# Optimization experiments

Measured on AMD Instinct MI355X. Metric: run time of the kernel, lower is better.

The kernel has to match this reference:

```python
import jax, jax.numpy as jnp
import numpy as np

# Model dims (match init_kwargs / input_specs)
T, N, E, F_IN, F_OUT, BW = 16, 50000, 131072, 64, 64, 3


def setup_inputs() -> dict:
    key = jax.random.key(0)
    ks = jax.random.split(key, 6)
    x = jax.random.normal(ks[0], (T, N, F_IN), dtype=jnp.float32)
    M = jax.random.normal(ks[1], (T, T), dtype=jnp.float32)
    adj_rows = jax.random.randint(ks[2], (T, E), 0, N, dtype=jnp.int32)
    adj_cols = jax.random.randint(ks[3], (T, E), 0, N, dtype=jnp.int32)
    adj_vals = jax.random.uniform(ks[4], (T, E), dtype=jnp.float32)
    lim = float(np.sqrt(6.0 / (F_IN + F_OUT)))  # xavier_uniform
    weight = jax.random.uniform(ks[5], (F_IN, F_OUT), minval=-lim, maxval=lim, dtype=jnp.float32)
    return {"x": x, "M": M, "adj_vals": adj_vals, "weight": weight,
            "adj_rows": adj_rows, "adj_cols": adj_cols}


def _spmm(vals, rows, cols, x):
    # COO sparse [N,N] @ dense [N,F]: gather source rows, scatter-add to dest rows.
    return jax.ops.segment_sum(vals[:, None] * x[cols], rows, num_segments=x.shape[0])


def reference(x, M, adj_vals, weight, adj_rows, adj_cols):
    Tn, Nn, F = x.shape
    # Xt = M @ X (full M, as in compute_AtXt)
    Xt = (M @ x.reshape(Tn, -1)).reshape(Tn, Nn, F)
    k_idx = jnp.arange(Tn)
    AtXt = jnp.zeros((Tn, Nn, F), dtype=x.dtype)
    # Banded combination: At[k] = sum_{d=0}^{BW-1, k-d>=0} M[k, k-d] * A[k-d]
    # so At[k] @ Xt[k] = sum_d M[k,k-d] * (A[k-d] @ Xt[k])  -- avoids materializing At.
    for d in range(BW):
        j = k_idx - d
        valid = j >= 0
        jc = jnp.maximum(j, 0)
        w = jnp.where(valid, M[k_idx, jc], 0.0)  # [T] banded weights
        contrib = jax.vmap(_spmm)(adj_vals[jc], adj_rows[jc], adj_cols[jc], Xt)  # [T,N,F]
        AtXt = AtXt + w[:, None, None] * contrib
    # dropout is identity in eval mode; final dense projection
    return AtXt @ weight  # [T, N, F_OUT]
```

## Files before the change

kernel.cpp:

```cpp
#include <hip/hip_runtime.h>

#define TT 16
#define NN 50000
#define FF 64
#define EE 131072
#define NEDGE (TT*EE)
#define RPB 32
#define NRANGE ((NN + RPB - 1) / RPB)
#define NSUB 8
#define BCAP 256
#define NBUCK (NRANGE*NSUB)
#define SLOTS (NSUB*BCAP)
#define EMAX 1791
#define TAILI (EMAX*2)
#define NTILES 6250
#define K1BLKS 1563
#define APPBLKS (NEDGE/256)

typedef __attribute__((ext_vector_type(8))) short bf16x8;
typedef __attribute__((ext_vector_type(4))) short bf16x4;
typedef __attribute__((ext_vector_type(4))) float f32x4;
typedef __attribute__((ext_vector_type(2))) int   i32x2;
typedef __attribute__((ext_vector_type(2))) unsigned u32x2;

__device__ __forceinline__ unsigned pack2bf(float a, float b) {
    unsigned ua = __float_as_uint(a) + 0x8000u;
    unsigned ub = __float_as_uint(b) + 0x8000u;
    return __builtin_amdgcn_perm(ub, ua, 0x07060302u);
}
__device__ __forceinline__ float lo16f(unsigned u) { return __uint_as_float(u << 16); }
__device__ __forceinline__ float hi16f(unsigned u) { return __uint_as_float(u & 0xFFFF0000u); }

union U8 { unsigned u[4]; bf16x8 v; };
union U4 { unsigned u[2]; bf16x4 v; };

__device__ __forceinline__ f32x4 mfma16x16x16bf16(bf16x4 a, bf16x4 b, f32x4 c) {
#if __has_builtin(__builtin_amdgcn_mfma_f32_16x16x16bf16_1k)
    return __builtin_amdgcn_mfma_f32_16x16x16bf16_1k(a, b, c, 0, 0, 0);
#elif __has_builtin(__builtin_amdgcn_mfma_f32_16x16x16_bf16)
    return __builtin_amdgcn_mfma_f32_16x16x16_bf16(a, b, c, 0, 0, 0);
#else
    f32x4 d;
    asm volatile("v_mfma_f32_16x16x16_bf16 %0, %1, %2, %3\n\ts_nop 7\n\ts_nop 7"
                 : "=&v"(d) : "v"(a), "v"(b), "v"(c));
    return d;
#endif
}

__global__ void k1_append(
    const float* __restrict__ x, const float* __restrict__ M,
    const float* __restrict__ W, unsigned short* __restrict__ Yt,
    const int* __restrict__ rows, const int* __restrict__ cols,
    const float* __restrict__ vals, int* __restrict__ bcnt,
    i32x2* __restrict__ btmp)
{
    __shared__ __align__(16) char lds[2][16384];

    if (blockIdx.x < K1BLKS) {
        const int tid  = threadIdx.x;
        const int wid  = tid >> 6;
        const int lane = tid & 63;
        const int col  = lane & 15;
        const int grp  = lane >> 4;

        bf16x8 bw[2][4];
#pragma unroll
        for (int q = 0; q < 2; ++q)
#pragma unroll
            for (int t = 0; t < 4; ++t) {
                U8 w8;
#pragma unroll
                for (int p = 0; p < 4; ++p)
                    w8.u[p] = pack2bf(W[(q*32 + grp*8 + 2*p)*FF + t*16 + col],
                                      W[(q*32 + grp*8 + 2*p + 1)*FF + t*16 + col]);
                bw[q][t] = w8.v;
            }

        U4 m4;
        m4.u[0] = pack2bf(M[col*16 + grp*4 + 0], M[col*16 + grp*4 + 1]);
        m4.u[1] = pack2bf(M[col*16 + grp*4 + 2], M[col*16 + grp*4 + 3]);
        const bf16x4 mf = m4.v;
        const f32x4 zero = {0.f, 0.f, 0.f, 0.f};

#define STAGE(tt, buf)                                                        \
        {                                                                     \
            const int nb_ = (tt)*8;                                           \
            char* L_ = lds[buf];                                              \
            _Pragma("unroll")                                                 \
            for (int q = 0; q < 4; ++q) {                                     \
                const int s_ = wid*4 + q;                                     \
                const float* src_ = x + (size_t)s_*NN*FF + (size_t)nb_*FF + lane*8; \
                float4 lo_ = *reinterpret_cast<const float4*>(src_);          \
                float4 hi_ = *reinterpret_cast<const float4*>(src_ + 4);      \
                U8 pk_;                                                       \
                pk_.u[0] = pack2bf(lo_.x, lo_.y); pk_.u[1] = pack2bf(lo_.z, lo_.w); \
                pk_.u[2] = pack2bf(hi_.x, hi_.y); pk_.u[3] = pack2bf(hi_.z, hi_.w); \
                const int byte_ = (s_*1024 + lane*16) ^ ((s_ & 7) << 4);      \
                *reinterpret_cast<bf16x8*>(L_ + byte_) = pk_.v;               \
            }                                                                 \
        }

        const int t0 = blockIdx.x*4;
        if (t0 < NTILES) STAGE(t0, 0)

#pragma unroll
        for (int i = 0; i < 4; ++i) {
            const int t = t0 + i;
            if (t >= NTILES) break;
            __syncthreads();
            if (i + 1 < 4 && t + 1 < NTILES) STAGE(t + 1, (i + 1) & 1)

            const char* L = lds[i & 1];
#pragma unroll
            for (int h = 0; h < 2; ++h) {
                const int nloc = wid*2 + h;
                const int node = t*8 + nloc;
                const int base = (col*1024 + nloc*128) ;
                const int sw = (col & 7) << 4;
                bf16x8 a0 = *reinterpret_cast<const bf16x8*>(L + ((base + grp*16) ^ sw));
                bf16x8 a1 = *reinterpret_cast<const bf16x8*>(L + ((base + 64 + grp*16) ^ sw));

                f32x4 acc[4];
#pragma unroll
                for (int t2 = 0; t2 < 4; ++t2) acc[t2] = zero;
#pragma unroll
                for (int t2 = 0; t2 < 4; ++t2)
                    acc[t2] = __builtin_amdgcn_mfma_f32_16x16x32_bf16(a0, bw[0][t2], acc[t2], 0, 0, 0);
#pragma unroll
                for (int t2 = 0; t2 < 4; ++t2)
                    acc[t2] = __builtin_amdgcn_mfma_f32_16x16x32_bf16(a1, bw[1][t2], acc[t2], 0, 0, 0);

#pragma unroll
                for (int t2 = 0; t2 < 4; ++t2) {
                    U4 pb;
                    pb.u[0] = pack2bf(acc[t2][0], acc[t2][1]);
                    pb.u[1] = pack2bf(acc[t2][2], acc[t2][3]);
                    f32x4 y = mfma16x16x16bf16(pb.v, mf, zero);
                    u32x2 st;
                    st[0] = pack2bf(y[0], y[1]);
                    st[1] = pack2bf(y[2], y[3]);
                    *reinterpret_cast<u32x2*>(Yt + (size_t)node*1024 + col*64 + t2*16 + grp*4) = st;
                }
            }
        }
#undef STAGE
    } else {
        const int i = (blockIdx.x - K1BLKS)*256 + threadIdx.x;
        const int r = rows[i];
        const int j = i >> 17;
        const int b = (r >> 5)*NSUB + (blockIdx.x & 7);
        const int pos = atomicAdd(&bcnt[b], 1);
        if (pos < BCAP) {
            i32x2 e;
            e[0] = cols[i] | (((r & 31)*16 + j) << 16);
            e[1] = __float_as_int(vals[i]);
            btmp[(size_t)b*BCAP + pos] = e;
        }
    }
}

__global__ __launch_bounds__(256) void sort_kernel(
    const int* __restrict__ bcnt, i32x2* __restrict__ btmp)
{
    __shared__ i32x2 sbuf[SLOTS];
    __shared__ int scnt[512], soff[512], scur[512], pscan[256];

    const int tid = threadIdx.x;
    const int blk = blockIdx.x;
    i32x2* region = btmp + (size_t)blk*SLOTS;

    scnt[tid] = 0; scnt[tid + 256] = 0;
    __syncthreads();

    int bc[NSUB]; i32x2 ent[NSUB];
#pragma unroll
    for (int s = 0; s < NSUB; ++s) {
        int c = bcnt[blk*NSUB + s];
        bc[s] = c < BCAP ? c : BCAP;
    }
#pragma unroll
    for (int s = 0; s < NSUB; ++s)
        if (tid < bc[s]) {
            ent[s] = region[s*BCAP + tid];
            atomicAdd(&scnt[((unsigned)ent[s][0]) >> 16], 1);
        }
    __syncthreads();

    const int a0 = scnt[2*tid], a1 = scnt[2*tid + 1];
    const int ps = a0 + a1;
    pscan[tid] = ps;
    __syncthreads();
    for (int o = 1; o < 256; o <<= 1) {
        int v = (tid >= o) ? pscan[tid - o] : 0;
        __syncthreads();
        pscan[tid] += v;
        __syncthreads();
    }
    const int excl = pscan[tid] - ps;
    soff[2*tid] = excl;      soff[2*tid + 1] = excl + a0;
    scur[2*tid] = excl;      scur[2*tid + 1] = excl + a0;
    __syncthreads();

#pragma unroll
    for (int s = 0; s < NSUB; ++s)
        if (tid < bc[s]) {
            const int key = ((unsigned)ent[s][0]) >> 16;
            const int pos = atomicAdd(&scur[key], 1);
            i32x2 se; se[0] = ent[s][0] & 0xFFFF; se[1] = ent[s][1];
            sbuf[pos] = se;
        }
    __syncthreads();

    const int total = soff[511] + scnt[511];
    const int lim = total < EMAX ? total : EMAX;
    for (int i = tid; i < lim; i += 256) region[i] = sbuf[i];
    int* tail = (int*)region + TAILI;
    tail[tid] = soff[tid];
    tail[tid + 256] = soff[tid + 256];
    if (tid == 0) tail[512] = lim;
}

template<int J>
__device__ __forceinline__ void k2_batch(int p0, int nj, int sbase, int esub, int fq,
    const i32x2* eb, const unsigned short* __restrict__ Yt,
    const float* __restrict__ M, f32x4* acc)
{
    const int p = p0 + esub;
    const bool act = p < nj;
    const int li = act ? (sbase + p) : 0;
    const i32x2 ent = eb[li];
    const float v = act ? __int_as_float(ent[1]) : 0.f;
    const int node = act ? ent[0] : 0;
    const unsigned short* yb = Yt + (size_t)node*1024 + J*64 + fq*4;
    {
        const u32x2 uv = *reinterpret_cast<const u32x2*>(yb);
        const float wv = M[J*17] * v;
        acc[J][0] = fmaf(wv, lo16f(uv[0]), acc[J][0]);
        acc[J][1] = fmaf(wv, hi16f(uv[0]), acc[J][1]);
        acc[J][2] = fmaf(wv, lo16f(uv[1]), acc[J][2]);
        acc[J][3] = fmaf(wv, hi16f(uv[1]), acc[J][3]);
    }
    if constexpr (J < 15) {
        const u32x2 uv = *reinterpret_cast<const u32x2*>(yb + 64);
        const float wv = M[J*17 + 16] * v;
        acc[J+1][0] = fmaf(wv, lo16f(uv[0]), acc[J+1][0]);
        acc[J+1][1] = fmaf(wv, hi16f(uv[0]), acc[J+1][1]);
        acc[J+1][2] = fmaf(wv, lo16f(uv[1]), acc[J+1][2]);
        acc[J+1][3] = fmaf(wv, hi16f(uv[1]), acc[J+1][3]);
    }
    if constexpr (J < 14) {
        const u32x2 uv = *reinterpret_cast<const u32x2*>(yb + 128);
        const float wv = M[J*17 + 32] * v;
        acc[J+2][0] = fmaf(wv, lo16f(uv[0]), acc[J+2][0]);
        acc[J+2][1] = fmaf(wv, hi16f(uv[0]), acc[J+2][1]);
        acc[J+2][2] = fmaf(wv, lo16f(uv[1]), acc[J+2][2]);
        acc[J+2][3] = fmaf(wv, hi16f(uv[1]), acc[J+2][3]);
    }
}

__global__ __launch_bounds__(256) void k2_gather(
    const unsigned short* __restrict__ Yt, const float* __restrict__ M,
    const i32x2* __restrict__ btmp, float* __restrict__ out)
{
    __shared__ i32x2 ebuf[4][128];
    const int tid  = threadIdx.x;
    const int wid  = tid >> 6;
    const int lane = tid & 63;
    const int esub = lane >> 4;
    const int fq   = lane & 15;
    const int r   = blockIdx.x*4 + wid;
    const int blk = r >> 5;
    const int rl  = r & 31;

    const i32x2* region = btmp + (size_t)blk*SLOTS;
    const int* tail = (const int*)region + TAILI;
    int o_l = 0;
    if (lane < 17) o_l = tail[rl*16 + lane];
    int off[17];
#pragma unroll
    for (int j = 0; j < 17; ++j) off[j] = __builtin_amdgcn_readlane(o_l, j);
    int ntot = off[16] - off[0];
    ntot = ntot < 128 ? ntot : 128;
    const i32x2* rowsrc = region + off[0];

    i32x2* eb = ebuf[wid];
    if (lane < ntot)      eb[lane]      = rowsrc[lane];
    if (lane + 64 < ntot) eb[lane + 64] = rowsrc[lane + 64];

    int c[16], sb[16];
#pragma unroll
    for (int j = 0; j < 16; ++j) {
        c[j]  = off[j+1] - off[j];
        sb[j] = off[j] - off[0];
    }

    f32x4 acc[16];
#pragma unroll
    for (int k = 0; k < 16; ++k) acc[k] = (f32x4){0.f, 0.f, 0.f, 0.f};

#define P1(J) k2_batch<J>(0, c[J], sb[J], esub, fq, eb, Yt, M, acc);
    P1(0)  P1(1)  P1(2)  P1(3)  P1(4)  P1(5)  P1(6)  P1(7)
    P1(8)  P1(9)  P1(10) P1(11) P1(12) P1(13) P1(14) P1(15)
#undef P1
#define P2(J) for (int p0 = 4; p0 < c[J]; p0 += 4) \
        k2_batch<J>(p0, c[J], sb[J], esub, fq, eb, Yt, M, acc);
    P2(0)  P2(1)  P2(2)  P2(3)  P2(4)  P2(5)  P2(6)  P2(7)
    P2(8)  P2(9)  P2(10) P2(11) P2(12) P2(13) P2(14) P2(15)
#undef P2

#pragma unroll
    for (int k = 0; k < 16; ++k) {
#pragma unroll
        for (int u = 0; u < 4; ++u) {
            acc[k][u] += __shfl_xor(acc[k][u], 16);
            acc[k][u] += __shfl_xor(acc[k][u], 32);
        }
    }
    if (esub == 0) {
#pragma unroll
        for (int k = 0; k < 16; ++k) {
            *reinterpret_cast<f32x4*>(out + ((size_t)k*NN + r)*FF + fq*4) = acc[k];
        }
    }
}

extern "C" void kernel_launch(void* const* d_in, const int* in_sizes, int n_in,
                              void* d_out, int out_size, void* d_ws, size_t ws_size,
                              hipStream_t stream) {
    (void)in_sizes; (void)n_in; (void)out_size; (void)ws_size;
    const float* x     = (const float*)d_in[0];
    const float* M     = (const float*)d_in[1];
    const float* avals = (const float*)d_in[2];
    const float* W     = (const float*)d_in[3];
    const int*   arows = (const int*)d_in[4];
    const int*   acols = (const int*)d_in[5];
    float* out = (float*)d_out;

    char* ws = (char*)d_ws;
    size_t o = 0;
    unsigned short* Yt = (unsigned short*)(ws + o); o += (size_t)TT*NN*FF*2;
    o = (o + 255) & ~(size_t)255;
    int* bcnt = (int*)(ws + o); o += (size_t)NBUCK*4;  o = (o + 255) & ~(size_t)255;
    i32x2* btmp = (i32x2*)(ws + o);

    (void)hipMemsetAsync(bcnt, 0, (size_t)NBUCK*4, stream);
    hipLaunchKernelGGL(k1_append, dim3(K1BLKS + APPBLKS), dim3(256), 0, stream,
                       x, M, W, Yt, arows, acols, avals, bcnt, btmp);
    hipLaunchKernelGGL(sort_kernel, dim3(NRANGE), dim3(256), 0, stream, bcnt, btmp);
    hipLaunchKernelGGL(k2_gather, dim3(12500), dim3(256), 0, stream, Yt, M, btmp, out);
}
```

Measured before the change: 329.4 us.

## Vectorize edge append to four edges per thread and schedule it first

The edge bucketing branch now handles four edges per thread with 128-bit loads of rows, cols and vals, cutting its block count from 8192 to 2048, and these blocks are placed ahead of the dense transform blocks in the grid. The dense branch drops LDS double buffering in favour of a single buffer with stage, sync, compute, sync, which halves shared memory per block and may raise occupancy but gives up overlap of global loads with MFMA work. The sub-bucket choice still depends on blockIdx.x & 7, so contention on the atomics changes with the new block grouping.

New measurement: 347.7 us. 1.06x slower.

```diff
diff --git a/kernel.cpp b/kernel.cpp
--- a/kernel.cpp
+++ b/kernel.cpp
@@ -14,8 +14,8 @@
 #define EMAX 1791
 #define TAILI (EMAX*2)
 #define NTILES 6250
+#define APP4BLKS 2048
 #define K1BLKS 1563
-#define APPBLKS (NEDGE/256)
 
 typedef __attribute__((ext_vector_type(8))) short bf16x8;
 typedef __attribute__((ext_vector_type(4))) short bf16x4;
@@ -54,9 +54,34 @@
     const float* __restrict__ vals, int* __restrict__ bcnt,
     i32x2* __restrict__ btmp)
 {
-    __shared__ __align__(16) char lds[2][16384];
-
-    if (blockIdx.x < K1BLKS) {
+    __shared__ __align__(16) char lds[16384];
+
+    if (blockIdx.x < APP4BLKS) {
+        const int i0 = blockIdx.x*1024 + threadIdx.x*4;
+        const int4 r4 = *reinterpret_cast<const int4*>(rows + i0);
+        const int4 c4 = *reinterpret_cast<const int4*>(cols + i0);
+        const float4 v4 = *reinterpret_cast<const float4*>(vals + i0);
+        int rr[4] = {r4.x, r4.y, r4.z, r4.w};
+        int cc[4] = {c4.x, c4.y, c4.z, c4.w};
+        float vv[4] = {v4.x, v4.y, v4.z, v4.w};
+        int pos[4], bb[4];
+#pragma unroll
+        for (int e = 0; e < 4; ++e) {
+            bb[e] = (rr[e] >> 5)*NSUB + (blockIdx.x & 7);
+            pos[e] = atomicAdd(&bcnt[bb[e]], 1);
+        }
+#pragma unroll
+        for (int e = 0; e < 4; ++e) {
+            if (pos[e] < BCAP) {
+                const int j = (i0 + e) >> 17;
+                i32x2 ent;
+                ent[0] = cc[e] | (((rr[e] & 31)*16 + j) << 16);
+                ent[1] = __float_as_int(vv[e]);
+                btmp[(size_t)bb[e]*BCAP + pos[e]] = ent;
+            }
+        }
+    } else {
+        const int blk  = blockIdx.x - APP4BLKS;
         const int tid  = threadIdx.x;
         const int wid  = tid >> 6;
         const int lane = tid & 63;
@@ -82,10 +107,9 @@
         const bf16x4 mf = m4.v;
         const f32x4 zero = {0.f, 0.f, 0.f, 0.f};
 
-#define STAGE(tt, buf)                                                        \
+#define STAGE(tt)                                                             \
         {                                                                     \
             const int nb_ = (tt)*8;                                           \
-            char* L_ = lds[buf];                                              \
             _Pragma("unroll")                                                 \
             for (int q = 0; q < 4; ++q) {                                     \
                 const int s_ = wid*4 + q;                                     \
@@ -96,29 +120,26 @@
                 pk_.u[0] = pack2bf(lo_.x, lo_.y); pk_.u[1] = pack2bf(lo_.z, lo_.w); \
                 pk_.u[2] = pack2bf(hi_.x, hi_.y); pk_.u[3] = pack2bf(hi_.z, hi_.w); \
                 const int byte_ = (s_*1024 + lane*16) ^ ((s_ & 7) << 4);      \
-                *reinterpret_cast<bf16x8*>(L_ + byte_) = pk_.v;               \
+                *reinterpret_cast<bf16x8*>(lds + byte_) = pk_.v;              \
             }                                                                 \
         }
 
-        const int t0 = blockIdx.x*4;
-        if (t0 < NTILES) STAGE(t0, 0)
-
+        const int t0 = blk*4;
 #pragma unroll
         for (int i = 0; i < 4; ++i) {
             const int t = t0 + i;
             if (t >= NTILES) break;
+            STAGE(t)
             __syncthreads();
-            if (i + 1 < 4 && t + 1 < NTILES) STAGE(t + 1, (i + 1) & 1)
-
-            const char* L = lds[i & 1];
+
 #pragma unroll
             for (int h = 0; h < 2; ++h) {
                 const int nloc = wid*2 + h;
                 const int node = t*8 + nloc;
-                const int base = (col*1024 + nloc*128) ;
+                const int base = col*1024 + nloc*128;
                 const int sw = (col & 7) << 4;
-                bf16x8 a0 = *reinterpret_cast<const bf16x8*>(L + ((base + grp*16) ^ sw));
-                bf16x8 a1 = *reinterpret_cast<const bf16x8*>(L + ((base + 64 + grp*16) ^ sw));
+                bf16x8 a0 = *reinterpret_cast<const bf16x8*>(lds + ((base + grp*16) ^ sw));
+                bf16x8 a1 = *reinterpret_cast<const bf16x8*>(lds + ((base + 64 + grp*16) ^ sw));
 
                 f32x4 acc[4];
 #pragma unroll
@@ -142,20 +163,9 @@
                     *reinterpret_cast<u32x2*>(Yt + (size_t)node*1024 + col*64 + t2*16 + grp*4) = st;
                 }
             }
+            __syncthreads();
         }
 #undef STAGE
-    } else {
-        const int i = (blockIdx.x - K1BLKS)*256 + threadIdx.x;
-        const int r = rows[i];
-        const int j = i >> 17;
-        const int b = (r >> 5)*NSUB + (blockIdx.x & 7);
-        const int pos = atomicAdd(&bcnt[b], 1);
-        if (pos < BCAP) {
-            i32x2 e;
-            e[0] = cols[i] | (((r & 31)*16 + j) << 16);
-            e[1] = __float_as_int(vals[i]);
-            btmp[(size_t)b*BCAP + pos] = e;
-        }
     }
 }
 
@@ -344,7 +354,7 @@
     i32x2* btmp = (i32x2*)(ws + o);
 
     (void)hipMemsetAsync(bcnt, 0, (size_t)NBUCK*4, stream);
-    hipLaunchKernelGGL(k1_append, dim3(K1BLKS + APPBLKS), dim3(256), 0, stream,
+    hipLaunchKernelGGL(k1_append, dim3(APP4BLKS + K1BLKS), dim3(256), 0, stream,
                        x, M, W, Yt, arows, acols, avals, bcnt, btmp);
     hipLaunchKernelGGL(sort_kernel, dim3(NRANGE), dim3(256), 0, stream, bcnt, btmp);
     hipLaunchKernelGGL(k2_gather, dim3(12500), dim3(256), 0, stream, Yt, M, btmp, out);
```

## Split gather kernel into two launches over output time halves

Applied to the files above, without the earlier changes.

The gather kernel, which kept 16 output-time accumulators per lane, is split into two templated launches that each produce 8 output time steps. Each launch processes only the source time steps that feed its half, with time steps 6 and 7 read by both. The aim is to lower register pressure and raise occupancy. In exchange, edge lists and offsets are read twice, overlapping source rows are gathered twice, and there is an extra launch.

Measured after the change: 421.0 us. +27.8%, slower.

```diff
diff --git a/kernel.cpp b/kernel.cpp
--- a/kernel.cpp
+++ b/kernel.cpp
@@ -115,7 +115,7 @@
             for (int h = 0; h < 2; ++h) {
                 const int nloc = wid*2 + h;
                 const int node = t*8 + nloc;
-                const int base = (col*1024 + nloc*128) ;
+                const int base = col*1024 + nloc*128;
                 const int sw = (col & 7) << 4;
                 bf16x8 a0 = *reinterpret_cast<const bf16x8*>(L + ((base + grp*16) ^ sw));
                 bf16x8 a1 = *reinterpret_cast<const bf16x8*>(L + ((base + 64 + grp*16) ^ sw));
@@ -220,7 +220,7 @@
     if (tid == 0) tail[512] = lim;
 }
 
-template<int J>
+template<int J, int KLO>
 __device__ __forceinline__ void k2_batch(int p0, int nj, int sbase, int esub, int fq,
     const i32x2* eb, const unsigned short* __restrict__ Yt,
     const float* __restrict__ M, f32x4* acc)
@@ -231,38 +231,29 @@
     const i32x2 ent = eb[li];
     const float v = act ? __int_as_float(ent[1]) : 0.f;
     const int node = act ? ent[0] : 0;
-    const unsigned short* yb = Yt + (size_t)node*1024 + J*64 + fq*4;
-    {
-        const u32x2 uv = *reinterpret_cast<const u32x2*>(yb);
-        const float wv = M[J*17] * v;
-        acc[J][0] = fmaf(wv, lo16f(uv[0]), acc[J][0]);
-        acc[J][1] = fmaf(wv, hi16f(uv[0]), acc[J][1]);
-        acc[J][2] = fmaf(wv, lo16f(uv[1]), acc[J][2]);
-        acc[J][3] = fmaf(wv, hi16f(uv[1]), acc[J][3]);
-    }
-    if constexpr (J < 15) {
-        const u32x2 uv = *reinterpret_cast<const u32x2*>(yb + 64);
-        const float wv = M[J*17 + 16] * v;
-        acc[J+1][0] = fmaf(wv, lo16f(uv[0]), acc[J+1][0]);
-        acc[J+1][1] = fmaf(wv, hi16f(uv[0]), acc[J+1][1]);
-        acc[J+1][2] = fmaf(wv, lo16f(uv[1]), acc[J+1][2]);
-        acc[J+1][3] = fmaf(wv, hi16f(uv[1]), acc[J+1][3]);
-    }
-    if constexpr (J < 14) {
-        const u32x2 uv = *reinterpret_cast<const u32x2*>(yb + 128);
-        const float wv = M[J*17 + 32] * v;
-        acc[J+2][0] = fmaf(wv, lo16f(uv[0]), acc[J+2][0]);
-        acc[J+2][1] = fmaf(wv, hi16f(uv[0]), acc[J+2][1]);
-        acc[J+2][2] = fmaf(wv, lo16f(uv[1]), acc[J+2][2]);
-        acc[J+2][3] = fmaf(wv, hi16f(uv[1]), acc[J+2][3]);
-    }
-}
-
-__global__ __launch_bounds__(256) void k2_gather(
+    const unsigned short* yb = Yt + (size_t)node*1024 + fq*4;
+#pragma unroll
+    for (int d = 0; d < 3; ++d) {
+        if (J + d >= KLO && J + d < KLO + 8 && J + d < 16) {
+            const int K = J + d;
+            const u32x2 uv = *reinterpret_cast<const u32x2*>(yb + K*64);
+            const float wv = M[K*16 + J] * v;
+            acc[K - KLO][0] = fmaf(wv, lo16f(uv[0]), acc[K - KLO][0]);
+            acc[K - KLO][1] = fmaf(wv, hi16f(uv[0]), acc[K - KLO][1]);
+            acc[K - KLO][2] = fmaf(wv, lo16f(uv[1]), acc[K - KLO][2]);
+            acc[K - KLO][3] = fmaf(wv, hi16f(uv[1]), acc[K - KLO][3]);
+        }
+    }
+}
+
+template<int KLO>
+__global__ __launch_bounds__(256) void k2_half(
     const unsigned short* __restrict__ Yt, const float* __restrict__ M,
     const i32x2* __restrict__ btmp, float* __restrict__ out)
 {
-    __shared__ i32x2 ebuf[4][128];
+    constexpr int JLO = (KLO == 0) ? 0 : 6;
+    constexpr int JHI = (KLO == 0) ? 7 : 15;
+    __shared__ i32x2 ebuf[4][96];
     const int tid  = threadIdx.x;
     const int wid  = tid >> 6;
     const int lane = tid & 63;
@@ -279,9 +270,9 @@
     int off[17];
 #pragma unroll
     for (int j = 0; j < 17; ++j) off[j] = __builtin_amdgcn_readlane(o_l, j);
-    int ntot = off[16] - off[0];
-    ntot = ntot < 128 ? ntot : 128;
-    const i32x2* rowsrc = region + off[0];
+    int ntot = off[JHI + 1] - off[JLO];
+    ntot = ntot < 96 ? ntot : 96;
+    const i32x2* rowsrc = region + off[JLO];
 
     i32x2* eb = ebuf[wid];
     if (lane < ntot)      eb[lane]      = rowsrc[lane];
@@ -289,27 +280,30 @@
 
     int c[16], sb[16];
 #pragma unroll
-    for (int j = 0; j < 16; ++j) {
+    for (int j = JLO; j <= JHI; ++j) {
         c[j]  = off[j+1] - off[j];
-        sb[j] = off[j] - off[0];
-    }
-
-    f32x4 acc[16];
-#pragma unroll
-    for (int k = 0; k < 16; ++k) acc[k] = (f32x4){0.f, 0.f, 0.f, 0.f};
-
-#define P1(J) k2_batch<J>(0, c[J], sb[J], esub, fq, eb, Yt, M, acc);
-    P1(0)  P1(1)  P1(2)  P1(3)  P1(4)  P1(5)  P1(6)  P1(7)
-    P1(8)  P1(9)  P1(10) P1(11) P1(12) P1(13) P1(14) P1(15)
+        sb[j] = off[j] - off[JLO];
+    }
+
+    f32x4 acc[8];
+#pragma unroll
+    for (int k = 0; k < 8; ++k) acc[k] = (f32x4){0.f, 0.f, 0.f, 0.f};
+
+#define P1(J) k2_batch<J,KLO>(0, c[J], sb[J], esub, fq, eb, Yt, M, acc);
+#define P2(J) for (int p0 = 4; p0 < c[J]; p0 += 4) \
+        k2_batch<J,KLO>(p0, c[J], sb[J], esub, fq, eb, Yt, M, acc);
+    if constexpr (KLO == 0) {
+        P1(0) P1(1) P1(2) P1(3) P1(4) P1(5) P1(6) P1(7)
+        P2(0) P2(1) P2(2) P2(3) P2(4) P2(5) P2(6) P2(7)
+    } else {
+        P1(6) P1(7) P1(8) P1(9) P1(10) P1(11) P1(12) P1(13) P1(14) P1(15)
+        P2(6) P2(7) P2(8) P2(9) P2(10) P2(11) P2(12) P2(13) P2(14) P2(15)
+    }
 #undef P1
-#define P2(J) for (int p0 = 4; p0 < c[J]; p0 += 4) \
-        k2_batch<J>(p0, c[J], sb[J], esub, fq, eb, Yt, M, acc);
-    P2(0)  P2(1)  P2(2)  P2(3)  P2(4)  P2(5)  P2(6)  P2(7)
-    P2(8)  P2(9)  P2(10) P2(11) P2(12) P2(13) P2(14) P2(15)
 #undef P2
 
 #pragma unroll
-    for (int k = 0; k < 16; ++k) {
+    for (int k = 0; k < 8; ++k) {
 #pragma unroll
         for (int u = 0; u < 4; ++u) {
             acc[k][u] += __shfl_xor(acc[k][u], 16);
@@ -318,8 +312,8 @@
     }
     if (esub == 0) {
 #pragma unroll
-        for (int k = 0; k < 16; ++k) {
-            *reinterpret_cast<f32x4*>(out + ((size_t)k*NN + r)*FF + fq*4) = acc[k];
+        for (int k = 0; k < 8; ++k) {
+            *reinterpret_cast<f32x4*>(out + ((size_t)(KLO + k)*NN + r)*FF + fq*4) = acc[k];
         }
     }
 }
@@ -347,5 +341,6 @@
     hipLaunchKernelGGL(k1_append, dim3(K1BLKS + APPBLKS), dim3(256), 0, stream,
                        x, M, W, Yt, arows, acols, avals, bcnt, btmp);
     hipLaunchKernelGGL(sort_kernel, dim3(NRANGE), dim3(256), 0, stream, bcnt, btmp);
-    hipLaunchKernelGGL(k2_gather, dim3(12500), dim3(256), 0, stream, Yt, M, btmp, out);
-}
+    hipLaunchKernelGGL(k2_half<0>, dim3(12500), dim3(256), 0, stream, Yt, M, btmp, out);
+    hipLaunchKernelGGL(k2_half<8>, dim3(12500), dim3(256), 0, stream, Yt, M, btmp, out);
+}
```
